# Kernel optimization log

Measured on AMD Instinct MI355X. Metric: run time of the kernel, lower is better.

Reference implementation:

```python
import jax, jax.numpy as jnp
import numpy as np

N = 100000      # num nodes
F = 128         # node_features
HID = 32        # DCRNN out_channels (fixed in module)
E = 3200000     # num edges (avg degree 32)


def _gate_w(k, scale=0.05):
    # DConv weight shape (2, K=1, in_channels, out_channels); in = F + HID
    return (jax.random.normal(k, (2, 1, F + HID, HID), jnp.float32) * scale)


def setup_inputs() -> dict:
    key = jax.random.key(0)
    ks = jax.random.split(key, 10)
    x = jax.random.normal(ks[0], (N, F), jnp.float32)
    edge_index = jax.random.randint(ks[1], (2, E), 0, N, dtype=jnp.int64)
    edge_weight = jax.random.uniform(ks[2], (E,), jnp.float32)
    return {
        "x": x,
        "edge_index": edge_index,
        "edge_weight": edge_weight,
        "W_z": _gate_w(ks[3]), "b_z": jnp.zeros((HID,), jnp.float32),
        "W_r": _gate_w(ks[4]), "b_r": jnp.zeros((HID,), jnp.float32),
        "W_h": _gate_w(ks[5]), "b_h": jnp.zeros((HID,), jnp.float32),
        "W_lin": jax.random.normal(ks[6], (HID, 1), jnp.float32) * 0.1,
        "b_lin": jnp.zeros((1,), jnp.float32),
    }


def _dconv_k1(C, W, b):
    # torch_geometric_temporal DConv with K=1: only the k=0 (identity) term of
    # both forward/backward diffusion; the propagate branch requires K>1.
    # H = C @ W[0,0] + C @ W[1,0] + b
    return C @ (W[0, 0] + W[1, 0]) + b


def reference(x, edge_index, edge_weight, W_z, b_z, W_r, b_r, W_h, b_h, W_lin, b_lin):
    # DCRNN cell, hidden state H defaults to zeros. With K=1, edge_index and
    # edge_weight only feed dead degree/adjacency computations in the original.
    H0 = jnp.zeros((x.shape[0], HID), x.dtype)
    XH = jnp.concatenate([x, H0], axis=1)            # [N, F+HID]
    Z = jax.nn.sigmoid(_dconv_k1(XH, W_z, b_z))      # update gate [N, HID]
    R = jax.nn.sigmoid(_dconv_k1(XH, W_r, b_r))      # reset gate  [N, HID]
    XHR = jnp.concatenate([x, H0 * R], axis=1)
    H_tilde = jnp.tanh(_dconv_k1(XHR, W_h, b_h))     # candidate   [N, HID]
    H = Z * H0 + (1.0 - Z) * H_tilde
    h = jax.nn.relu(H)
    return h @ W_lin + b_lin                          # [N, 1]
```

## Files before the change

### kernel.cpp

```cpp
#include <hip/hip_runtime.h>

#define FEAT 128
#define HID 32
#define NPB 64
#define BLOCK 256

typedef __attribute__((ext_vector_type(8))) __bf16 bf16x8;
typedef __attribute__((ext_vector_type(8))) unsigned short ushortx8;
typedef __attribute__((ext_vector_type(4))) float floatx4;

static __device__ inline unsigned short f2bf(float f) {
    unsigned int u = __builtin_bit_cast(unsigned int, f);
    u += 0x7FFFu + ((u >> 16) & 1u);
    return (unsigned short)(u >> 16);
}
static __device__ inline float fsig(float v) {
    return __builtin_amdgcn_rcpf(1.f + __expf(-v));
}
static __device__ inline float ftanh(float v) {
    return 1.f - 2.f * __builtin_amdgcn_rcpf(__expf(2.f * v) + 1.f);
}

__global__ __launch_bounds__(BLOCK) void dcrnn_fused1(
    const float* __restrict__ x,
    const float* __restrict__ Wz, const float* __restrict__ Wh,
    const float* __restrict__ bz, const float* __restrict__ bh,
    const float* __restrict__ wl, const float* __restrict__ bl,
    float* __restrict__ out, int n_nodes)
{
    __shared__ unsigned short sX[NPB * FEAT];
    __shared__ unsigned short sW[64 * FEAT];

    const int tid = threadIdx.x;
    const long long node0 = (long long)blockIdx.x * NPB;

    #pragma unroll
    for (int p = 0; p < 4; ++p) {
        int idx8 = p * BLOCK + tid;
        int row = idx8 >> 4, k0 = (idx8 & 15) * 8;
        long long node = node0 + row;
        ushortx8 v = {0, 0, 0, 0, 0, 0, 0, 0};
        if (node < n_nodes) {
            const float4 a = *(const float4*)&x[node * FEAT + k0];
            const float4 b = *(const float4*)&x[node * FEAT + k0 + 4];
            v[0] = f2bf(a.x); v[1] = f2bf(a.y); v[2] = f2bf(a.z); v[3] = f2bf(a.w);
            v[4] = f2bf(b.x); v[5] = f2bf(b.y); v[6] = f2bf(b.z); v[7] = f2bf(b.w);
        }
        *(ushortx8*)&sX[row * FEAT + (k0 ^ ((row & 7) << 3))] = v;
    }

    {
        const int o4 = (tid & 7) * 4;
        const int kb = tid >> 3;
        #pragma unroll
        for (int kk = kb; kk < FEAT; kk += 32) {
            const float4 z0 = *(const float4*)&Wz[kk * HID + o4];
            const float4 z1 = *(const float4*)&Wz[5120 + kk * HID + o4];
            const float4 h0 = *(const float4*)&Wh[kk * HID + o4];
            const float4 h1 = *(const float4*)&Wh[5120 + kk * HID + o4];
            const float zs[4] = {z0.x + z1.x, z0.y + z1.y, z0.z + z1.z, z0.w + z1.w};
            const float hs[4] = {h0.x + h1.x, h0.y + h1.y, h0.z + h1.z, h0.w + h1.w};
            #pragma unroll
            for (int j = 0; j < 4; ++j) {
                const int rz = o4 + j;
                const int rh = rz + 32;
                sW[rz * FEAT + (kk ^ ((rz & 7) << 3))] = f2bf(zs[j]);
                sW[rh * FEAT + (kk ^ ((rh & 7) << 3))] = f2bf(hs[j]);
            }
        }
    }
    __syncthreads();

    const int w  = tid >> 6;
    const int l  = tid & 63;
    const int n0 = l & 15;
    const int g  = l >> 4;

    floatx4 acc[4] = {{0,0,0,0},{0,0,0,0},{0,0,0,0},{0,0,0,0}};

    #pragma unroll
    for (int s = 0; s < 4; ++s) {
        const int k0 = s * 32 + g * 8;
        const int ar = w * 16 + n0;
        bf16x8 afrag = __builtin_bit_cast(bf16x8,
            *(const ushortx8*)&sX[ar * FEAT + (k0 ^ ((ar & 7) << 3))]);
        #pragma unroll
        for (int nt = 0; nt < 4; ++nt) {
            const int br = nt * 16 + n0;
            bf16x8 bfrag = __builtin_bit_cast(bf16x8,
                *(const ushortx8*)&sW[br * FEAT + (k0 ^ ((br & 7) << 3))]);
            acc[nt] = __builtin_amdgcn_mfma_f32_16x16x32_bf16(afrag, bfrag, acc[nt], 0, 0, 0);
        }
    }

    const float bz0 = bz[n0], bz1 = bz[n0 + 16];
    const float bh0 = bh[n0], bh1 = bh[n0 + 16];
    const float wl0 = wl[n0], wl1 = wl[n0 + 16];
    const float blv = bl[0];

    float4 res;
    float* resp = &res.x;
    #pragma unroll
    for (int r = 0; r < 4; ++r) {
        float z0 = fsig(acc[0][r] + bz0);
        float z1 = fsig(acc[1][r] + bz1);
        float h0 = ftanh(acc[2][r] + bh0);
        float h1 = ftanh(acc[3][r] + bh1);
        float v0 = (1.f - z0) * h0; v0 = v0 > 0.f ? v0 : 0.f;
        float v1 = (1.f - z1) * h1; v1 = v1 > 0.f ? v1 : 0.f;
        float s = v0 * wl0 + v1 * wl1;
        s += __shfl_xor(s, 1);
        s += __shfl_xor(s, 2);
        s += __shfl_xor(s, 4);
        s += __shfl_xor(s, 8);
        resp[r] = s + blv;
    }
    if (n0 == 0) {
        long long m = node0 + w * 16 + g * 4;
        if (m < n_nodes) *(float4*)&out[m] = res;
    }
}

extern "C" void kernel_launch(void* const* d_in, const int* in_sizes, int n_in,
                              void* d_out, int out_size, void* d_ws, size_t ws_size,
                              hipStream_t stream) {
    const float* x    = (const float*)d_in[0];
    const float* Wz   = (const float*)d_in[3];
    const float* bz   = (const float*)d_in[4];
    const float* Wh   = (const float*)d_in[7];
    const float* bh   = (const float*)d_in[8];
    const float* Wlin = (const float*)d_in[9];
    const float* blin = (const float*)d_in[10];
    float* out = (float*)d_out;

    const int n_nodes = in_sizes[0] / FEAT;
    const int grid = (n_nodes + NPB - 1) / NPB;
    dcrnn_fused1<<<grid, BLOCK, 0, stream>>>(x, Wz, Wh, bz, bh, Wlin, blin, out, n_nodes);
}
```

Baseline: 20.13 us.

## Precompute MFMA weight fragments in prep kernel and load x directly to registers

A small prep kernel now sums and converts the two gate weight slices into bf16 in the exact MFMA B-fragment order, stored in the workspace. The main kernel drops shared memory and the block barrier: each lane loads its x row segments straight into registers, converts them to bf16 in place, and reads the pre-laid-out weight fragments with vector loads. This removes per-block redundant weight summation, LDS staging and synchronisation, and adds occupancy hints. The cost is a second kernel launch and more registers held per thread.

New measurement: 22.25 us. 1.11x slower.

```diff
diff --git a/kernel.cpp b/kernel.cpp
--- a/kernel.cpp
+++ b/kernel.cpp
@@ -21,76 +21,64 @@
     return 1.f - 2.f * __builtin_amdgcn_rcpf(__expf(2.f * v) + 1.f);
 }
 
-__global__ __launch_bounds__(BLOCK) void dcrnn_fused1(
+__global__ void prep_wfrag(const float* __restrict__ Wz,
+                           const float* __restrict__ Wh,
+                           unsigned short* __restrict__ wfrag) {
+    int e = blockIdx.x * blockDim.x + threadIdx.x;
+    if (e >= 16 * 64 * 8) return;
+    int j = e & 7, l = (e >> 3) & 63, f = e >> 9;
+    int nt = f & 3, s = f >> 2;
+    int k = s * 32 + (l >> 4) * 8 + j;
+    int o = nt * 16 + (l & 15);
+    const float* W = (o < HID) ? Wz : Wh;
+    int col = o & 31;
+    float v = W[k * HID + col] + W[5120 + k * HID + col];
+    wfrag[e] = f2bf(v);
+}
+
+__global__ __launch_bounds__(BLOCK, 3) void dcrnn_main(
     const float* __restrict__ x,
-    const float* __restrict__ Wz, const float* __restrict__ Wh,
+    const unsigned short* __restrict__ wfrag,
     const float* __restrict__ bz, const float* __restrict__ bh,
     const float* __restrict__ wl, const float* __restrict__ bl,
     float* __restrict__ out, int n_nodes)
 {
-    __shared__ unsigned short sX[NPB * FEAT];
-    __shared__ unsigned short sW[64 * FEAT];
-
     const int tid = threadIdx.x;
-    const long long node0 = (long long)blockIdx.x * NPB;
-
-    #pragma unroll
-    for (int p = 0; p < 4; ++p) {
-        int idx8 = p * BLOCK + tid;
-        int row = idx8 >> 4, k0 = (idx8 & 15) * 8;
-        long long node = node0 + row;
-        ushortx8 v = {0, 0, 0, 0, 0, 0, 0, 0};
-        if (node < n_nodes) {
-            const float4 a = *(const float4*)&x[node * FEAT + k0];
-            const float4 b = *(const float4*)&x[node * FEAT + k0 + 4];
-            v[0] = f2bf(a.x); v[1] = f2bf(a.y); v[2] = f2bf(a.z); v[3] = f2bf(a.w);
-            v[4] = f2bf(b.x); v[5] = f2bf(b.y); v[6] = f2bf(b.z); v[7] = f2bf(b.w);
-        }
-        *(ushortx8*)&sX[row * FEAT + (k0 ^ ((row & 7) << 3))] = v;
-    }
-
-    {
-        const int o4 = (tid & 7) * 4;
-        const int kb = tid >> 3;
-        #pragma unroll
-        for (int kk = kb; kk < FEAT; kk += 32) {
-            const float4 z0 = *(const float4*)&Wz[kk * HID + o4];
-            const float4 z1 = *(const float4*)&Wz[5120 + kk * HID + o4];
-            const float4 h0 = *(const float4*)&Wh[kk * HID + o4];
-            const float4 h1 = *(const float4*)&Wh[5120 + kk * HID + o4];
-            const float zs[4] = {z0.x + z1.x, z0.y + z1.y, z0.z + z1.z, z0.w + z1.w};
-            const float hs[4] = {h0.x + h1.x, h0.y + h1.y, h0.z + h1.z, h0.w + h1.w};
-            #pragma unroll
-            for (int j = 0; j < 4; ++j) {
-                const int rz = o4 + j;
-                const int rh = rz + 32;
-                sW[rz * FEAT + (kk ^ ((rz & 7) << 3))] = f2bf(zs[j]);
-                sW[rh * FEAT + (kk ^ ((rh & 7) << 3))] = f2bf(hs[j]);
-            }
-        }
-    }
-    __syncthreads();
-
     const int w  = tid >> 6;
     const int l  = tid & 63;
     const int n0 = l & 15;
     const int g  = l >> 4;
 
+    const long long node0 = (long long)blockIdx.x * NPB;
+    const long long row   = node0 + w * 16 + n0;
+    const long long rowc  = row < n_nodes ? row : (long long)(n_nodes - 1);
+    const float* xr = x + rowc * FEAT + g * 8;
+
+    float4 xa[4], xb[4];
+    #pragma unroll
+    for (int s = 0; s < 4; ++s) {
+        xa[s] = *(const float4*)(xr + s * 32);
+        xb[s] = *(const float4*)(xr + s * 32 + 4);
+    }
+    ushortx8 bfr[16];
+    #pragma unroll
+    for (int f = 0; f < 16; ++f)
+        bfr[f] = *(const ushortx8*)(wfrag + (f * 64 + l) * 8);
+
     floatx4 acc[4] = {{0,0,0,0},{0,0,0,0},{0,0,0,0},{0,0,0,0}};
 
     #pragma unroll
     for (int s = 0; s < 4; ++s) {
-        const int k0 = s * 32 + g * 8;
-        const int ar = w * 16 + n0;
-        bf16x8 afrag = __builtin_bit_cast(bf16x8,
-            *(const ushortx8*)&sX[ar * FEAT + (k0 ^ ((ar & 7) << 3))]);
+        ushortx8 av;
+        av[0] = f2bf(xa[s].x); av[1] = f2bf(xa[s].y);
+        av[2] = f2bf(xa[s].z); av[3] = f2bf(xa[s].w);
+        av[4] = f2bf(xb[s].x); av[5] = f2bf(xb[s].y);
+        av[6] = f2bf(xb[s].z); av[7] = f2bf(xb[s].w);
+        bf16x8 afrag = __builtin_bit_cast(bf16x8, av);
         #pragma unroll
-        for (int nt = 0; nt < 4; ++nt) {
-            const int br = nt * 16 + n0;
-            bf16x8 bfrag = __builtin_bit_cast(bf16x8,
-                *(const ushortx8*)&sW[br * FEAT + (k0 ^ ((br & 7) << 3))]);
-            acc[nt] = __builtin_amdgcn_mfma_f32_16x16x32_bf16(afrag, bfrag, acc[nt], 0, 0, 0);
-        }
+        for (int nt = 0; nt < 4; ++nt)
+            acc[nt] = __builtin_amdgcn_mfma_f32_16x16x32_bf16(
+                afrag, __builtin_bit_cast(bf16x8, bfr[s * 4 + nt]), acc[nt], 0, 0, 0);
     }
 
     const float bz0 = bz[n0], bz1 = bz[n0 + 16];
@@ -133,7 +121,12 @@
     const float* blin = (const float*)d_in[10];
     float* out = (float*)d_out;
 
+    unsigned short* wfrag = (unsigned short*)d_ws;
+
     const int n_nodes = in_sizes[0] / FEAT;
+
+    prep_wfrag<<<(16 * 64 * 8 + BLOCK - 1) / BLOCK, BLOCK, 0, stream>>>(Wz, Wh, wfrag);
+
     const int grid = (n_nodes + NPB - 1) / NPB;
-    dcrnn_fused1<<<grid, BLOCK, 0, stream>>>(x, Wz, Wh, bz, bh, Wlin, blin, out, n_nodes);
+    dcrnn_main<<<grid, BLOCK, 0, stream>>>(x, wfrag, bz, bh, Wlin, blin, out, n_nodes);
 }
```
